# Kernel tuning notes

Measured on AMD Instinct MI355X. Metric: run time of the kernel, lower is better.

The kernel has to match this reference:

```python
import jax, jax.numpy as jnp
import numpy as np

B, T, V, H = 1, 1024, 32000, 2048
NH, NKV, HD = 8, 4, 256
QS, KVS = NH * HD, NKV * HD
I, L = 8192, 2
SCALE = 256.0 ** -0.5          # query_pre_attn_scalar ** -0.5
ATTN_CAP, FINAL_CAP = 50.0, 30.0
WIN, EPS, THETA = 512, 1e-6, 10000.0
NEG = -2.3819763e38


def setup_inputs() -> dict:
    key = jax.random.key(0)
    ks = jax.random.split(key, 12)
    s = 0.02
    return {
        "tokens": jax.random.randint(ks[0], (B, T), 0, V, dtype=jnp.int32),
        "embed": jax.random.normal(ks[1], (V, H), jnp.float32) * s,
        "qkv_w": jax.random.normal(ks[2], (L, (NH + 2 * NKV) * HD, H), jnp.float32) * s,
        "o_w": jax.random.normal(ks[3], (L, H, NH * HD), jnp.float32) * s,
        "gate_w": jax.random.normal(ks[4], (L, I, H), jnp.float32) * s,
        "up_w": jax.random.normal(ks[5], (L, I, H), jnp.float32) * s,
        "down_w": jax.random.normal(ks[6], (L, H, I), jnp.float32) * s,
        "ln_in": jax.random.normal(ks[7], (L, H), jnp.float32) * s,   # RMSNorm weight (zeros-init offset)
        "ln_pa": jax.random.normal(ks[8], (L, H), jnp.float32) * s,
        "ln_pre": jax.random.normal(ks[9], (L, H), jnp.float32) * s,
        "ln_post": jax.random.normal(ks[10], (L, H), jnp.float32) * s,
        "ln_f": jax.random.normal(ks[11], (H,), jnp.float32) * s,
    }


def rmsnorm(x, w):
    x = x.astype(jnp.float32)
    n = x * jax.lax.rsqrt(jnp.mean(x * x, axis=-1, keepdims=True) + EPS)
    return n * (1.0 + w)  # add_unit_offset=True


def rope(x, cos, sin):
    # x: [B, T, N, HD]; split-half complex rotary as in apply_rotary_emb
    x1, x2 = jnp.split(x, 2, axis=-1)
    c = cos[None, :, None, :]
    s = sin[None, :, None, :]
    return jnp.concatenate([x1 * c - x2 * s, x1 * s + x2 * c], axis=-1)


def reference(tokens, embed, qkv_w, o_w, gate_w, up_w, down_w,
              ln_in, ln_pa, ln_pre, ln_post, ln_f):
    pos = jnp.arange(T)
    inv = 1.0 / (THETA ** (jnp.arange(0, HD, 2, dtype=jnp.float32) / HD))  # [HD/2]
    ang = pos.astype(jnp.float32)[:, None] * inv[None, :]
    cos, sin = jnp.cos(ang), jnp.sin(ang)

    i, j = pos[:, None], pos[None, :]
    causal = j <= i
    mask_global = jnp.where(causal, 0.0, NEG).astype(jnp.float32)
    mask_local = jnp.where(causal & (i - j < WIN), 0.0, NEG).astype(jnp.float32)
    masks = [mask_local, mask_global]  # layer 0: LOCAL_SLIDING, layer 1: GLOBAL

    x = embed[tokens] * jnp.sqrt(jnp.float32(H))  # Gemma embedding normalizer

    for l in range(L):
        h = rmsnorm(x, ln_in[l])
        qkv = jnp.einsum('bth,oh->bto', h, qkv_w[l])
        q = qkv[..., :QS].reshape(B, T, NH, HD)
        k = qkv[..., QS:QS + KVS].reshape(B, T, NKV, HD)
        v = qkv[..., QS + KVS:].reshape(B, T, NKV, HD)
        q = rope(q, cos, sin)
        k = rope(k, cos, sin)
        # prefill: kv_write_indices=arange(T) -> cache == current k/v
        k = jnp.repeat(k, NH // NKV, axis=2)  # GQA repeat_interleave over heads
        v = jnp.repeat(v, NH // NKV, axis=2)
        scores = jnp.einsum('bqhd,bkhd->bhqk', q * SCALE, k)
        scores = jnp.tanh(scores / ATTN_CAP) * ATTN_CAP
        scores = scores + masks[l][None, None]
        attn = jax.nn.softmax(scores.astype(jnp.float32), axis=-1)
        out = jnp.einsum('bhqk,bkhd->bqhd', attn, v).reshape(B, T, NH * HD)
        out = jnp.einsum('bto,ho->bth', out, o_w[l])
        x = x + rmsnorm(out, ln_pa[l])

        h = rmsnorm(x, ln_pre[l])
        gate = jax.nn.gelu(jnp.einsum('bth,ih->bti', h, gate_w[l]), approximate=True)
        up = jnp.einsum('bth,ih->bti', h, up_w[l])
        ff = jnp.einsum('bti,hi->bth', gate * up, down_w[l])
        x = x + rmsnorm(ff, ln_post[l])

    x = rmsnorm(x, ln_f)
    logits = jnp.einsum('bth,vh->btv', x, embed)
    logits = jnp.tanh(logits / FINAL_CAP) * FINAL_CAP  # final_logit_softcapping
    return logits
```

## Files before the change

### kernel.cpp

```cpp
#include <hip/hip_runtime.h>
#include <hip/hip_bf16.h>
#include <math.h>

typedef unsigned short u16;
typedef __attribute__((ext_vector_type(8))) short bf16x8;
typedef __attribute__((ext_vector_type(4))) float f32x4;
typedef __attribute__((ext_vector_type(4))) u16 u16x4;

#define T_SEQ 1024
#define HDIM  2048
#define NHEAD 8
#define NKVH  4
#define HSZ   256
#define ISZ   8192
#define NVOC  32000

#define GLDS(src, dst) __builtin_amdgcn_global_load_lds( \
    (const __attribute__((address_space(1))) void*)(src), \
    (__attribute__((address_space(3))) void*)(dst), 16, 0, 0)

__device__ __forceinline__ u16 f2bf(float f) {
    union { float f; unsigned u; } v; v.f = f;
    return (u16)((v.u + 0x7fffu + ((v.u >> 16) & 1u)) >> 16);
}

__device__ __forceinline__ float fast_tanh(float x) {
    float e = __expf(-2.0f * fabsf(x));
    float t = (1.0f - e) / (1.0f + e);
    return copysignf(t, x);
}

__global__ __launch_bounds__(256)
void cvt_bf16(const float* __restrict__ s, u16* __restrict__ d, long n4)
{
    for (long i = blockIdx.x * 256L + threadIdx.x; i < n4; i += (long)gridDim.x * 256) {
        f32x4 v = ((const f32x4*)s)[i];
        u16x4 o;
        o.x = f2bf(v.x); o.y = f2bf(v.y); o.z = f2bf(v.z); o.w = f2bf(v.w);
        ((u16x4*)d)[i] = o;
    }
}

template<int EPI>
__global__ __launch_bounds__(512, 1)
void gemm_dp(const u16* __restrict__ A, int lda,
             const u16* __restrict__ B, int ldb,
             float* __restrict__ C, int ldc, long sC, int K)
{
    extern __shared__ u16 lds[];
    const int t = threadIdx.x;
    const int lane = t & 63, wid = t >> 6;
    const int z = blockIdx.z;
    A += (long)z * K;
    B += (long)z * K;
    C += (long)z * sC;

    const int nwg = gridDim.x * gridDim.y;
    int flat = blockIdx.y * gridDim.x + blockIdx.x;
    {
        const int q = nwg >> 3, r = nwg & 7;
        const int xcd = flat & 7, loc = flat >> 3;
        flat = (xcd < r ? xcd * (q + 1) : r * (q + 1) + (xcd - r) * q) + loc;
    }
    const int gm = gridDim.y;
    const long m0 = (long)(flat % gm) * 128;
    const long n0 = (long)(flat / gm) * 256;

    const int sr = t >> 3;
    const int sl = ((t & 7) ^ (sr & 7)) * 8;
    const u16* gA0 = A + (m0 + sr)       * (long)lda + sl;
    const u16* gA1 = A + (m0 + 64 + sr)  * (long)lda + sl;
    const u16* gB0 = B + (n0 + sr)       * (long)ldb + sl;
    const u16* gB1 = B + (n0 + 64 + sr)  * (long)ldb + sl;
    const u16* gB2 = B + (n0 + 128 + sr) * (long)ldb + sl;
    const u16* gB3 = B + (n0 + 192 + sr) * (long)ldb + sl;

    auto stage = [&](int kt) {
        const long ko = (long)kt * 64;
        char* d = (char*)lds + (kt % 3) * 49152 + t * 16;
        GLDS(gA0 + ko, d);
        GLDS(gA1 + ko, d + 8192);
        GLDS(gB0 + ko, d + 16384);
        GLDS(gB1 + ko, d + 24576);
        GLDS(gB2 + ko, d + 32768);
        GLDS(gB3 + ko, d + 40960);
    };

    f32x4 acc[4][4] = {};
    const int fr = lane & 15, kq = lane >> 4;
    const int wm = wid >> 2, wn = wid & 3;
    const int ps0 = ((kq)     ^ (lane & 7)) * 8;
    const int ps1 = ((4 + kq) ^ (lane & 7)) * 8;

    const int KT = K >> 6;
    stage(0);
    if (KT > 1) stage(1);
    if (KT > 2) stage(2);

    for (int kt = 0; kt < KT; ++kt) {
        if (kt < KT - 2)       asm volatile("s_waitcnt vmcnt(12)" ::: "memory");
        else if (kt == KT - 2) asm volatile("s_waitcnt vmcnt(6)" ::: "memory");
        else                   asm volatile("s_waitcnt vmcnt(0)" ::: "memory");
        __builtin_amdgcn_s_barrier();

        const u16* Asl = lds + (kt % 3) * 24576;
        const u16* Bsl = Asl + 8192;
        #pragma unroll
        for (int kk = 0; kk < 2; ++kk) {
            const int ps = kk ? ps1 : ps0;
            bf16x8 af[4], bfv[4];
            #pragma unroll
            for (int mi = 0; mi < 4; ++mi)
                af[mi] = *(const bf16x8*)(Asl + (wm * 64 + mi * 16 + fr) * 64 + ps);
            #pragma unroll
            for (int ni = 0; ni < 4; ++ni)
                bfv[ni] = *(const bf16x8*)(Bsl + (wn * 64 + ni * 16 + fr) * 64 + ps);
            #pragma unroll
            for (int mi = 0; mi < 4; ++mi)
                #pragma unroll
                for (int ni = 0; ni < 4; ++ni)
                    acc[mi][ni] = __builtin_amdgcn_mfma_f32_16x16x32_bf16(
                        af[mi], bfv[ni], acc[mi][ni], 0, 0, 0);
        }
        __builtin_amdgcn_s_barrier();
        if (kt + 3 < KT) stage(kt + 3);
    }

    const int crb = kq * 4, ccol = fr;
    #pragma unroll
    for (int mi = 0; mi < 4; ++mi) {
        #pragma unroll
        for (int rr = 0; rr < 4; ++rr) {
            const long row = m0 + wm * 64 + mi * 16 + crb + rr;
            float* cp = C + row * ldc + n0 + wn * 64 + ccol;
            #pragma unroll
            for (int ni = 0; ni < 4; ++ni) {
                float v = acc[mi][ni][rr];
                if (EPI == 1) v = fast_tanh(v * (1.0f / 30.0f)) * 30.0f;
                cp[ni * 16] = v;
            }
        }
    }
}

template<int EPI, typename CT>
__global__ __launch_bounds__(256)
void gemm_bt(const u16* __restrict__ A, int lda, long sA,
             const u16* __restrict__ B, int ldb, long sB, int bshift,
             CT* __restrict__ C, int ldc, long sC, int K)
{
    __shared__ u16 As[128 * 32];
    __shared__ u16 Bs[128 * 32];
    const int tid = threadIdx.x;
    const int lane = tid & 63, wid = tid >> 6;
    const int z = blockIdx.z;
    A += (long)z * sA;
    B += (long)(z >> bshift) * sB;
    C += (long)z * sC;

    const int nwg = gridDim.x * gridDim.y;
    int flat = blockIdx.y * gridDim.x + blockIdx.x;
    {
        const int q = nwg >> 3, r = nwg & 7;
        const int xcd = flat & 7, loc = flat >> 3;
        flat = (xcd < r ? xcd * (q + 1) : r * (q + 1) + (xcd - r) * q) + loc;
    }
    const int gm = gridDim.y;
    const long m0 = (long)(flat % gm) * 128;
    const long n0 = (long)(flat / gm) * 128;

    f32x4 acc[4][4] = {};

    const int ar = tid >> 2, ac = (tid & 3) * 8;
    const u16* gA0 = A + (m0 + ar) * lda + ac;
    const u16* gB0 = B + (n0 + ar) * (long)ldb + ac;
    const long a64 = 64L * lda, b64 = 64L * ldb;

    const int fr = lane & 15, fk = (lane >> 4) * 8;
    const int wm = (wid >> 1) * 64, wn = (wid & 1) * 64;

    for (int k0 = 0; k0 < K; k0 += 32) {
        GLDS(gA0 + k0,       &As[tid * 8]);
        GLDS(gA0 + a64 + k0, &As[2048 + tid * 8]);
        GLDS(gB0 + k0,       &Bs[tid * 8]);
        GLDS(gB0 + b64 + k0, &Bs[2048 + tid * 8]);
        __syncthreads();
        bf16x8 af[4], bfv[4];
        #pragma unroll
        for (int mi = 0; mi < 4; ++mi)
            af[mi] = *(const bf16x8*)(&As[(wm + mi * 16 + fr) * 32 + fk]);
        #pragma unroll
        for (int ni = 0; ni < 4; ++ni)
            bfv[ni] = *(const bf16x8*)(&Bs[(wn + ni * 16 + fr) * 32 + fk]);
        #pragma unroll
        for (int mi = 0; mi < 4; ++mi)
            #pragma unroll
            for (int ni = 0; ni < 4; ++ni)
                acc[mi][ni] = __builtin_amdgcn_mfma_f32_16x16x32_bf16(
                    af[mi], bfv[ni], acc[mi][ni], 0, 0, 0);
        __syncthreads();
    }

    const int crb = (lane >> 4) * 4, ccol = lane & 15;
    #pragma unroll
    for (int mi = 0; mi < 4; ++mi) {
        #pragma unroll
        for (int rr = 0; rr < 4; ++rr) {
            const long row = m0 + wm + mi * 16 + crb + rr;
            CT* cp = C + row * ldc + n0 + wn + ccol;
            #pragma unroll
            for (int ni = 0; ni < 4; ++ni) {
                float v = acc[mi][ni][rr];
                if (EPI == 1) v = fast_tanh(v * (1.0f / 30.0f)) * 30.0f;
                if constexpr (sizeof(CT) == 2) cp[ni * 16] = f2bf(v);
                else                           cp[ni * 16] = v;
            }
        }
    }
}

__global__ __launch_bounds__(256)
void embed_scale(const int* __restrict__ tok, const float* __restrict__ emb,
                 float* __restrict__ x)
{
    const int t = blockIdx.x, tid = threadIdx.x;
    const long src = (long)tok[t] * HDIM;
    f32x4 a = *(const f32x4*)(emb + src + tid * 8);
    f32x4 b = *(const f32x4*)(emb + src + tid * 8 + 4);
    a *= 45.254834f; b *= 45.254834f;
    *(f32x4*)(x + (long)t * HDIM + tid * 8) = a;
    *(f32x4*)(x + (long)t * HDIM + tid * 8 + 4) = b;
}

__device__ __forceinline__ float block_sum(float v, float* red) {
    #pragma unroll
    for (int o = 32; o; o >>= 1) v += __shfl_xor(v, o);
    const int tid = threadIdx.x;
    if ((tid & 63) == 0) red[tid >> 6] = v;
    __syncthreads();
    return red[0] + red[1] + red[2] + red[3];
}

__global__ __launch_bounds__(256)
void rmsnorm_bf16(const float* __restrict__ x, const float* __restrict__ w,
                  u16* __restrict__ out)
{
    __shared__ float red[4];
    const int t = blockIdx.x, tid = threadIdx.x;
    const float* row = x + (long)t * HDIM;
    f32x4 a = *(const f32x4*)(row + tid * 8);
    f32x4 b = *(const f32x4*)(row + tid * 8 + 4);
    float ss = a.x*a.x + a.y*a.y + a.z*a.z + a.w*a.w
             + b.x*b.x + b.y*b.y + b.z*b.z + b.w*b.w;
    ss = block_sum(ss, red);
    const float r = rsqrtf(ss * (1.0f / HDIM) + 1e-6f);
    f32x4 wa = *(const f32x4*)(w + tid * 8);
    f32x4 wb = *(const f32x4*)(w + tid * 8 + 4);
    u16x4 o0, o1;
    o0.x = f2bf(a.x * r * (1.0f + wa.x)); o0.y = f2bf(a.y * r * (1.0f + wa.y));
    o0.z = f2bf(a.z * r * (1.0f + wa.z)); o0.w = f2bf(a.w * r * (1.0f + wa.w));
    o1.x = f2bf(b.x * r * (1.0f + wb.x)); o1.y = f2bf(b.y * r * (1.0f + wb.y));
    o1.z = f2bf(b.z * r * (1.0f + wb.z)); o1.w = f2bf(b.w * r * (1.0f + wb.w));
    *(u16x4*)(out + (long)t * HDIM + tid * 8) = o0;
    *(u16x4*)(out + (long)t * HDIM + tid * 8 + 4) = o1;
}

__global__ __launch_bounds__(256)
void add_rmsnorm(float* __restrict__ x, const float* __restrict__ y,
                 const float* __restrict__ w, int nsplit, long stride)
{
    __shared__ float red[4];
    const int t = blockIdx.x, tid = threadIdx.x;
    const float* yr = y + (long)t * HDIM;
    f32x4 a = *(const f32x4*)(yr + tid * 8);
    f32x4 b = *(const f32x4*)(yr + tid * 8 + 4);
    for (int s = 1; s < nsplit; ++s) {
        a += *(const f32x4*)(yr + s * stride + tid * 8);
        b += *(const f32x4*)(yr + s * stride + tid * 8 + 4);
    }
    float ss = a.x*a.x + a.y*a.y + a.z*a.z + a.w*a.w
             + b.x*b.x + b.y*b.y + b.z*b.z + b.w*b.w;
    ss = block_sum(ss, red);
    const float r = rsqrtf(ss * (1.0f / HDIM) + 1e-6f);
    f32x4 wa = *(const f32x4*)(w + tid * 8);
    f32x4 wb = *(const f32x4*)(w + tid * 8 + 4);
    float* xr = x + (long)t * HDIM;
    f32x4 xa = *(const f32x4*)(xr + tid * 8);
    f32x4 xb = *(const f32x4*)(xr + tid * 8 + 4);
    xa.x += a.x * r * (1.0f + wa.x); xa.y += a.y * r * (1.0f + wa.y);
    xa.z += a.z * r * (1.0f + wa.z); xa.w += a.w * r * (1.0f + wa.w);
    xb.x += b.x * r * (1.0f + wb.x); xb.y += b.y * r * (1.0f + wb.y);
    xb.z += b.z * r * (1.0f + wb.z); xb.w += b.w * r * (1.0f + wb.w);
    *(f32x4*)(xr + tid * 8) = xa;
    *(f32x4*)(xr + tid * 8 + 4) = xb;
}

#define QKV_STRIDE (1024L * 4096)

__global__ __launch_bounds__(256)
void qkv_post(const float* __restrict__ qkv, u16* __restrict__ qb,
              u16* __restrict__ kb)
{
    const int t = blockIdx.x, tid = threadIdx.x;
    const float* row = qkv + (long)t * 4096;
    const float ft = (float)t;
    #pragma unroll
    for (int it = 0; it < 4; ++it) {
        const int p = tid + it * 256;
        const int nh = p >> 7, d = p & 127;
        const float inv = powf(10000.0f, -(float)d * (1.0f / 128.0f));
        const float ang = ft * inv;
        const float c = cosf(ang), s = sinf(ang);
        const int i1 = nh * 256 + d, i2 = i1 + 128;
        const float x1 = row[i1] + row[i1 + QKV_STRIDE];
        const float x2 = row[i2] + row[i2 + QKV_STRIDE];
        const long ob = ((long)nh * T_SEQ + t) * HSZ;
        qb[ob + d]       = f2bf((x1 * c - x2 * s) * 0.0625f);
        qb[ob + 128 + d] = f2bf((x1 * s + x2 * c) * 0.0625f);
    }
    #pragma unroll
    for (int it = 0; it < 2; ++it) {
        const int p = tid + it * 256;
        const int kv = p >> 7, d = p & 127;
        const float inv = powf(10000.0f, -(float)d * (1.0f / 128.0f));
        const float ang = ft * inv;
        const float c = cosf(ang), s = sinf(ang);
        const int i1 = 2048 + kv * 256 + d, i2 = i1 + 128;
        const float x1 = row[i1] + row[i1 + QKV_STRIDE];
        const float x2 = row[i2] + row[i2 + QKV_STRIDE];
        const long ob = ((long)kv * T_SEQ + t) * HSZ;
        kb[ob + d]       = f2bf(x1 * c - x2 * s);
        kb[ob + 128 + d] = f2bf(x1 * s + x2 * c);
    }
}

__global__ __launch_bounds__(256)
void v_transpose(const float* __restrict__ qkvb, u16* __restrict__ vT)
{
    __shared__ u16 tile[64][65];
    const int t0 = blockIdx.x * 64, d0 = blockIdx.y * 64, kv = blockIdx.z;
    const int lane = threadIdx.x & 63, w = threadIdx.x >> 6;
    #pragma unroll
    for (int i = 0; i < 16; ++i) {
        const int t = w * 16 + i;
        const long idx = (long)(t0 + t) * 4096 + 3072 + kv * 256 + d0 + lane;
        tile[t][lane] = f2bf(qkvb[idx] + qkvb[idx + QKV_STRIDE]);
    }
    __syncthreads();
    #pragma unroll
    for (int i = 0; i < 16; ++i) {
        const int d = w * 16 + i;
        vT[((long)kv * HSZ + d0 + d) * T_SEQ + t0 + lane] = tile[lane][d];
    }
}

__global__ __launch_bounds__(256)
void softmax_mask(const float* __restrict__ sc, u16* __restrict__ pr, int win)
{
    __shared__ float redm[4], reds[4];
    const int i = blockIdx.x, h = blockIdx.y, tid = threadIdx.x;
    const long base = ((long)h * T_SEQ + i) * T_SEQ;
    f32x4 sv = *(const f32x4*)(sc + base + tid * 4);
    float vals[4];
    #pragma unroll
    for (int j = 0; j < 4; ++j) {
        const int col = tid * 4 + j;
        const float s = fast_tanh(sv[j] * 0.02f) * 50.0f;
        const bool valid = (col <= i) && ((i - col) < win);
        vals[j] = valid ? s : -3.0e38f;
    }
    float m = fmaxf(fmaxf(vals[0], vals[1]), fmaxf(vals[2], vals[3]));
    #pragma unroll
    for (int o = 32; o; o >>= 1) m = fmaxf(m, __shfl_xor(m, o));
    if ((tid & 63) == 0) redm[tid >> 6] = m;
    __syncthreads();
    m = fmaxf(fmaxf(redm[0], redm[1]), fmaxf(redm[2], redm[3]));
    float sum = 0.0f;
    #pragma unroll
    for (int j = 0; j < 4; ++j) { vals[j] = __expf(vals[j] - m); sum += vals[j]; }
    #pragma unroll
    for (int o = 32; o; o >>= 1) sum += __shfl_xor(sum, o);
    if ((tid & 63) == 0) reds[tid >> 6] = sum;
    __syncthreads();
    sum = reds[0] + reds[1] + reds[2] + reds[3];
    const float inv = 1.0f / sum;
    u16x4 o4;
    #pragma unroll
    for (int j = 0; j < 4; ++j) o4[j] = f2bf(vals[j] * inv);
    *(u16x4*)(pr + base + tid * 4) = o4;
}

__global__ __launch_bounds__(256)
void mul_gelu(const float* __restrict__ g, const float* __restrict__ u,
              u16* __restrict__ p)
{
    const int n4 = (T_SEQ * ISZ) / 4;
    for (int i = blockIdx.x * 256 + threadIdx.x; i < n4; i += gridDim.x * 256) {
        f32x4 gv = ((const f32x4*)g)[i];
        f32x4 uv = ((const f32x4*)u)[i];
        u16x4 w;
        #pragma unroll
        for (int j = 0; j < 4; ++j) {
            const float xg = gv[j];
            const float tt = fast_tanh(0.79788456f * (xg + 0.044715f * xg * xg * xg));
            w[j] = f2bf(0.5f * xg * (1.0f + tt) * uv[j]);
        }
        ((u16x4*)p)[i] = w;
    }
}

extern "C" void kernel_launch(void* const* d_in, const int* in_sizes, int n_in,
                              void* d_out, int out_size, void* d_ws, size_t ws_size,
                              hipStream_t stream)
{
    (void)in_sizes; (void)n_in; (void)out_size; (void)ws_size;
    const int*   tokens = (const int*)  d_in[0];
    const float* emb    = (const float*)d_in[1];
    const float* qkv_w  = (const float*)d_in[2];
    const float* o_w    = (const float*)d_in[3];
    const float* gate_w = (const float*)d_in[4];
    const float* up_w   = (const float*)d_in[5];
    const float* down_w = (const float*)d_in[6];
    const float* ln_in  = (const float*)d_in[7];
    const float* ln_pa  = (const float*)d_in[8];
    const float* ln_pre = (const float*)d_in[9];
    const float* ln_post= (const float*)d_in[10];
    const float* ln_f   = (const float*)d_in[11];
    float* logits = (float*)d_out;

    char* base = (char*)d_ws;
    size_t off = 0;
    auto alloc = [&](size_t b) { char* p = base + off; off += (b + 255) & ~(size_t)255; return p; };

    float* x    = (float*)alloc((size_t)T_SEQ * HDIM * 4);
    u16*   hb   = (u16*)  alloc((size_t)T_SEQ * HDIM * 2);
    u16*   qb   = (u16*)  alloc((size_t)NHEAD * T_SEQ * HSZ * 2);
    u16*   kb   = (u16*)  alloc((size_t)NKVH * T_SEQ * HSZ * 2);
    u16*   vT   = (u16*)  alloc((size_t)NKVH * HSZ * T_SEQ * 2);
    u16*   ao   = (u16*)  alloc((size_t)T_SEQ * HDIM * 2);
    u16*   pb   = (u16*)  alloc((size_t)T_SEQ * ISZ * 2);
    char*  big  = alloc((size_t)2 * T_SEQ * ISZ * 4);
    float* P    = (float*)big;
    float* sc   = (float*)big;
    u16*   pr   = (u16*)(big + (size_t)NHEAD * T_SEQ * T_SEQ * 4);
    float* gb   = (float*)big;
    float* ub   = (float*)(big + (size_t)T_SEQ * ISZ * 4);
    u16*   wb   = (u16*)  alloc((size_t)NVOC * HDIM * 2);

    const size_t LDSB = 3 * 49152;
    const long s2048 = 1024L * 2048;

    embed_scale<<<T_SEQ, 256, 0, stream>>>(tokens, emb, x);
    for (int l = 0; l < 2; ++l) {
        rmsnorm_bf16<<<T_SEQ, 256, 0, stream>>>(x, ln_in + l * HDIM, hb);
        cvt_bf16<<<2048, 256, 0, stream>>>(qkv_w + (size_t)l * 4096 * HDIM, wb, 4096L * HDIM / 4);
        gemm_dp<0><<<dim3(16, 8, 2), 512, LDSB, stream>>>(
            hb, HDIM, wb, HDIM, P, 4096, QKV_STRIDE, 1024);
        qkv_post<<<T_SEQ, 256, 0, stream>>>(P, qb, kb);
        v_transpose<<<dim3(16, 4, 4), 256, 0, stream>>>(P, vT);
        gemm_bt<0, float><<<dim3(8, 8, NHEAD), 256, 0, stream>>>(
            qb, HSZ, (long)T_SEQ * HSZ, kb, HSZ, (long)T_SEQ * HSZ, 1,
            sc, T_SEQ, (long)T_SEQ * T_SEQ, HSZ);
        softmax_mask<<<dim3(T_SEQ, NHEAD, 1), 256, 0, stream>>>(
            sc, pr, l == 0 ? 512 : (1 << 30));
        gemm_bt<0, u16><<<dim3(2, 8, NHEAD), 256, 0, stream>>>(
            pr, T_SEQ, (long)T_SEQ * T_SEQ, vT, T_SEQ, (long)HSZ * T_SEQ, 1,
            ao, HDIM, (long)HSZ, T_SEQ);
        cvt_bf16<<<2048, 256, 0, stream>>>(o_w + (size_t)l * HDIM * HDIM, wb, (long)HDIM * HDIM / 4);
        gemm_dp<0><<<dim3(8, 8, 4), 512, LDSB, stream>>>(
            ao, HDIM, wb, HDIM, P, HDIM, s2048, 512);
        add_rmsnorm<<<T_SEQ, 256, 0, stream>>>(x, P, ln_pa + l * HDIM, 4, s2048);
        rmsnorm_bf16<<<T_SEQ, 256, 0, stream>>>(x, ln_pre + l * HDIM, hb);
        cvt_bf16<<<2048, 256, 0, stream>>>(gate_w + (size_t)l * ISZ * HDIM, wb, (long)ISZ * HDIM / 4);
        gemm_dp<0><<<dim3(32, 8, 1), 512, LDSB, stream>>>(
            hb, HDIM, wb, HDIM, gb, ISZ, 0, HDIM);
        cvt_bf16<<<2048, 256, 0, stream>>>(up_w + (size_t)l * ISZ * HDIM, wb, (long)ISZ * HDIM / 4);
        gemm_dp<0><<<dim3(32, 8, 1), 512, LDSB, stream>>>(
            hb, HDIM, wb, HDIM, ub, ISZ, 0, HDIM);
        mul_gelu<<<2048, 256, 0, stream>>>(gb, ub, pb);
        cvt_bf16<<<2048, 256, 0, stream>>>(down_w + (size_t)l * HDIM * ISZ, wb, (long)HDIM * ISZ / 4);
        gemm_dp<0><<<dim3(8, 8, 4), 512, LDSB, stream>>>(
            pb, ISZ, wb, ISZ, P, HDIM, s2048, 2048);
        add_rmsnorm<<<T_SEQ, 256, 0, stream>>>(x, P, ln_post + l * HDIM, 4, s2048);
    }
    rmsnorm_bf16<<<T_SEQ, 256, 0, stream>>>(x, ln_f, hb);
    cvt_bf16<<<2048, 256, 0, stream>>>(emb, wb, (long)NVOC * HDIM / 4);
    gemm_dp<1><<<dim3(125, 8, 1), 512, LDSB, stream>>>(
        hb, HDIM, wb, HDIM, logits, NVOC, 0, HDIM);
}
```

Before: 901.3 us.

## Fuse fp32-to-bf16 weight conversion into GEMM B-tile loading

Removes the separate cvt_bf16 passes over every weight matrix. The GEMM now loads fp32 B tiles into registers, packs them to bf16 with v_cvt_pk_bf16_f32, and writes them swizzled into LDS, while A tiles keep using global_load_lds. The pipeline drops from three LDS stages to two, with register double-buffering for B. This saves a full read and write of the weights per call, but each GEMM block now reads twice the B bytes and has a shallower pipeline with extra VGPR pressure.

Result: slower. 989.5 us (+9.8%).

```diff
diff --git a/kernel.cpp b/kernel.cpp
--- a/kernel.cpp
+++ b/kernel.cpp
@@ -6,6 +6,7 @@
 typedef __attribute__((ext_vector_type(8))) short bf16x8;
 typedef __attribute__((ext_vector_type(4))) float f32x4;
 typedef __attribute__((ext_vector_type(4))) u16 u16x4;
+typedef __attribute__((ext_vector_type(2))) unsigned u32x2;
 
 #define T_SEQ 1024
 #define HDIM  2048
@@ -24,27 +25,22 @@
     return (u16)((v.u + 0x7fffu + ((v.u >> 16) & 1u)) >> 16);
 }
 
+__device__ __forceinline__ unsigned cvt_pk_bf16(float a, float b) {
+    unsigned r;
+    asm("v_cvt_pk_bf16_f32 %0, %1, %2" : "=v"(r) : "v"(a), "v"(b));
+    return r;
+}
+
 __device__ __forceinline__ float fast_tanh(float x) {
     float e = __expf(-2.0f * fabsf(x));
     float t = (1.0f - e) / (1.0f + e);
     return copysignf(t, x);
 }
 
-__global__ __launch_bounds__(256)
-void cvt_bf16(const float* __restrict__ s, u16* __restrict__ d, long n4)
-{
-    for (long i = blockIdx.x * 256L + threadIdx.x; i < n4; i += (long)gridDim.x * 256) {
-        f32x4 v = ((const f32x4*)s)[i];
-        u16x4 o;
-        o.x = f2bf(v.x); o.y = f2bf(v.y); o.z = f2bf(v.z); o.w = f2bf(v.w);
-        ((u16x4*)d)[i] = o;
-    }
-}
-
 template<int EPI>
 __global__ __launch_bounds__(512, 1)
 void gemm_dp(const u16* __restrict__ A, int lda,
-             const u16* __restrict__ B, int ldb,
+             const float* __restrict__ B, int ldb,
              float* __restrict__ C, int ldc, long sC, int K)
 {
     extern __shared__ u16 lds[];
@@ -66,25 +62,14 @@
     const long m0 = (long)(flat % gm) * 128;
     const long n0 = (long)(flat / gm) * 256;
 
-    const int sr = t >> 3;
-    const int sl = ((t & 7) ^ (sr & 7)) * 8;
-    const u16* gA0 = A + (m0 + sr)       * (long)lda + sl;
-    const u16* gA1 = A + (m0 + 64 + sr)  * (long)lda + sl;
-    const u16* gB0 = B + (n0 + sr)       * (long)ldb + sl;
-    const u16* gB1 = B + (n0 + 64 + sr)  * (long)ldb + sl;
-    const u16* gB2 = B + (n0 + 128 + sr) * (long)ldb + sl;
-    const u16* gB3 = B + (n0 + 192 + sr) * (long)ldb + sl;
-
-    auto stage = [&](int kt) {
-        const long ko = (long)kt * 64;
-        char* d = (char*)lds + (kt % 3) * 49152 + t * 16;
-        GLDS(gA0 + ko, d);
-        GLDS(gA1 + ko, d + 8192);
-        GLDS(gB0 + ko, d + 16384);
-        GLDS(gB1 + ko, d + 24576);
-        GLDS(gB2 + ko, d + 32768);
-        GLDS(gB3 + ko, d + 40960);
-    };
+    const int asr = t >> 3;
+    const int asl = ((t & 7) ^ (asr & 7)) * 8;
+    const u16* gA0 = A + (m0 + asr)      * (long)lda + asl;
+    const u16* gA1 = A + (m0 + 64 + asr) * (long)lda + asl;
+
+    const float* gB = B + (n0 + (t >> 4)) * (long)ldb + (t & 15) * 4;
+    const long bstep = 32L * ldb;
+    const int boff = ((((t >> 1) & 7) ^ ((t >> 4) & 7)) << 4) + (t & 1) * 8;
 
     f32x4 acc[4][4] = {};
     const int fr = lane & 15, kq = lane >> 4;
@@ -93,17 +78,37 @@
     const int ps1 = ((4 + kq) ^ (lane & 7)) * 8;
 
     const int KT = K >> 6;
-    stage(0);
-    if (KT > 1) stage(1);
-    if (KT > 2) stage(2);
-
-    for (int kt = 0; kt < KT; ++kt) {
-        if (kt < KT - 2)       asm volatile("s_waitcnt vmcnt(12)" ::: "memory");
-        else if (kt == KT - 2) asm volatile("s_waitcnt vmcnt(6)" ::: "memory");
-        else                   asm volatile("s_waitcnt vmcnt(0)" ::: "memory");
+
+    auto stageA = [&](int kt) {
+        char* d = (char*)lds + (kt & 1) * 49152 + t * 16;
+        const long ko = (long)kt * 64;
+        GLDS(gA0 + ko, d);
+        GLDS(gA1 + ko, d + 8192);
+    };
+    auto loadB = [&](int kt, f32x4 (&R)[8]) {
+        const float* p = gB + (long)kt * 64;
+        #pragma unroll
+        for (int j = 0; j < 8; ++j) R[j] = *(const f32x4*)(p + j * bstep);
+    };
+    auto commitB = [&](int kt, f32x4 (&R)[8]) {
+        char* bb = (char*)lds + (kt & 1) * 49152 + 16384 + boff;
+        #pragma unroll
+        for (int j = 0; j < 8; ++j) {
+            u32x2 w;
+            w.x = cvt_pk_bf16(R[j].x, R[j].y);
+            w.y = cvt_pk_bf16(R[j].z, R[j].w);
+            *(u32x2*)(bb + (j * 32 + (t >> 4)) * 128) = w;
+        }
+    };
+    auto step = [&](int kt, f32x4 (&Rld)[8], f32x4 (&Rcm)[8]) {
+        if (kt + 1 < KT) asm volatile("s_waitcnt vmcnt(8)" ::: "memory");
+        else             asm volatile("s_waitcnt vmcnt(0)" ::: "memory");
+        asm volatile("s_waitcnt lgkmcnt(0)" ::: "memory");
         __builtin_amdgcn_s_barrier();
-
-        const u16* Asl = lds + (kt % 3) * 24576;
+        if (kt + 1 < KT) stageA(kt + 1);
+        if (kt + 2 < KT) loadB(kt + 2, Rld);
+
+        const u16* Asl = lds + (kt & 1) * 24576;
         const u16* Bsl = Asl + 8192;
         #pragma unroll
         for (int kk = 0; kk < 2; ++kk) {
@@ -122,8 +127,23 @@
                     acc[mi][ni] = __builtin_amdgcn_mfma_f32_16x16x32_bf16(
                         af[mi], bfv[ni], acc[mi][ni], 0, 0, 0);
         }
-        __builtin_amdgcn_s_barrier();
-        if (kt + 3 < KT) stage(kt + 3);
+        if (kt + 1 < KT) {
+            if (kt + 2 < KT) asm volatile("s_waitcnt vmcnt(10)" ::: "memory");
+            else             asm volatile("s_waitcnt vmcnt(2)" ::: "memory");
+            commitB(kt + 1, Rcm);
+        }
+    };
+
+    f32x4 R0[8], R1[8];
+    loadB(0, R0);
+    asm volatile("s_waitcnt vmcnt(0)" ::: "memory");
+    commitB(0, R0);
+    stageA(0);
+    loadB(1, R1);
+
+    for (int kt = 0; kt < KT; kt += 2) {
+        step(kt,     R0, R1);
+        step(kt + 1, R1, R0);
     }
 
     const int crb = kq * 4, ccol = fr;
@@ -445,17 +465,15 @@
     u16*   pr   = (u16*)(big + (size_t)NHEAD * T_SEQ * T_SEQ * 4);
     float* gb   = (float*)big;
     float* ub   = (float*)(big + (size_t)T_SEQ * ISZ * 4);
-    u16*   wb   = (u16*)  alloc((size_t)NVOC * HDIM * 2);
-
-    const size_t LDSB = 3 * 49152;
+
+    const size_t LDSB = 2 * 49152;
     const long s2048 = 1024L * 2048;
 
     embed_scale<<<T_SEQ, 256, 0, stream>>>(tokens, emb, x);
     for (int l = 0; l < 2; ++l) {
         rmsnorm_bf16<<<T_SEQ, 256, 0, stream>>>(x, ln_in + l * HDIM, hb);
-        cvt_bf16<<<2048, 256, 0, stream>>>(qkv_w + (size_t)l * 4096 * HDIM, wb, 4096L * HDIM / 4);
         gemm_dp<0><<<dim3(16, 8, 2), 512, LDSB, stream>>>(
-            hb, HDIM, wb, HDIM, P, 4096, QKV_STRIDE, 1024);
+            hb, HDIM, qkv_w + (size_t)l * 4096 * HDIM, HDIM, P, 4096, QKV_STRIDE, 1024);
         qkv_post<<<T_SEQ, 256, 0, stream>>>(P, qb, kb);
         v_transpose<<<dim3(16, 4, 4), 256, 0, stream>>>(P, vT);
         gemm_bt<0, float><<<dim3(8, 8, NHEAD), 256, 0, stream>>>(
@@ -466,25 +484,20 @@
         gemm_bt<0, u16><<<dim3(2, 8, NHEAD), 256, 0, stream>>>(
             pr, T_SEQ, (long)T_SEQ * T_SEQ, vT, T_SEQ, (long)HSZ * T_SEQ, 1,
             ao, HDIM, (long)HSZ, T_SEQ);
-        cvt_bf16<<<2048, 256, 0, stream>>>(o_w + (size_t)l * HDIM * HDIM, wb, (long)HDIM * HDIM / 4);
         gemm_dp<0><<<dim3(8, 8, 4), 512, LDSB, stream>>>(
-            ao, HDIM, wb, HDIM, P, HDIM, s2048, 512);
+            ao, HDIM, o_w + (size_t)l * HDIM * HDIM, HDIM, P, HDIM, s2048, 512);
         add_rmsnorm<<<T_SEQ, 256, 0, stream>>>(x, P, ln_pa + l * HDIM, 4, s2048);
         rmsnorm_bf16<<<T_SEQ, 256, 0, stream>>>(x, ln_pre + l * HDIM, hb);
-        cvt_bf16<<<2048, 256, 0, stream>>>(gate_w + (size_t)l * ISZ * HDIM, wb, (long)ISZ * HDIM / 4);
         gemm_dp<0><<<dim3(32, 8, 1), 512, LDSB, stream>>>(
-            hb, HDIM, wb, HDIM, gb, ISZ, 0, HDIM);
-        cvt_bf16<<<2048, 256, 0, stream>>>(up_w + (size_t)l * ISZ * HDIM, wb, (long)ISZ * HDIM / 4);
+            hb, HDIM, gate_w + (size_t)l * ISZ * HDIM, HDIM, gb, ISZ, 0, HDIM);
         gemm_dp<0><<<dim3(32, 8, 1), 512, LDSB, stream>>>(
-            hb, HDIM, wb, HDIM, ub, ISZ, 0, HDIM);
+            hb, HDIM, up_w + (size_t)l * ISZ * HDIM, HDIM, ub, ISZ, 0, HDIM);
         mul_gelu<<<2048, 256, 0, stream>>>(gb, ub, pb);
-        cvt_bf16<<<2048, 256, 0, stream>>>(down_w + (size_t)l * HDIM * ISZ, wb, (long)HDIM * ISZ / 4);
         gemm_dp<0><<<dim3(8, 8, 4), 512, LDSB, stream>>>(
-            pb, ISZ, wb, ISZ, P, HDIM, s2048, 2048);
+            pb, ISZ, down_w + (size_t)l * HDIM * ISZ, ISZ, P, HDIM, s2048, 2048);
         add_rmsnorm<<<T_SEQ, 256, 0, stream>>>(x, P, ln_post + l * HDIM, 4, s2048);
     }
     rmsnorm_bf16<<<T_SEQ, 256, 0, stream>>>(x, ln_f, hb);
-    cvt_bf16<<<2048, 256, 0, stream>>>(emb, wb, (long)NVOC * HDIM / 4);
     gemm_dp<1><<<dim3(125, 8, 1), 512, LDSB, stream>>>(
-        hb, HDIM, wb, HDIM, logits, NVOC, 0, HDIM);
-}
+        hb, HDIM, emb, HDIM, logits, NVOC, 0, HDIM);
+}
```

## Switch GEMMs to 256x256 tiles with interleaved 8-wave schedule and more split-K

Applied to the files above, without the earlier changes.

Replaces the 128x256 triple-buffered GEMM with a 256x256 double-buffered kernel that interleaves LDS fragment loads, global-to-LDS prefetch and MFMA clusters in four phases per K step, using barriers and s_setprio. Split-K factors are raised for the QKV, o-proj, down-proj and gate/up GEMMs to keep enough workgroups, with the reduction kernels summing 4 or 8 slices. The gate/up elementwise step is split into gelu_reduce and mul_reduce so both can reuse the single scratch buffer. The aim is higher arithmetic intensity per tile and better MFMA issue; the cost is extra split-K partial traffic and an intermediate bf16 rounding of the gelu output.

After: 1.004 ms. +11.4%, slower.

```diff
diff --git a/kernel.cpp b/kernel.cpp
--- a/kernel.cpp
+++ b/kernel.cpp
@@ -23,11 +23,18 @@
     union { float f; unsigned u; } v; v.f = f;
     return (u16)((v.u + 0x7fffu + ((v.u >> 16) & 1u)) >> 16);
 }
+__device__ __forceinline__ float bf2f(u16 h) {
+    union { unsigned u; float f; } v; v.u = (unsigned)h << 16; return v.f;
+}
 
 __device__ __forceinline__ float fast_tanh(float x) {
     float e = __expf(-2.0f * fabsf(x));
     float t = (1.0f - e) / (1.0f + e);
     return copysignf(t, x);
+}
+
+__device__ __forceinline__ f32x4 mfma16(bf16x8 a, bf16x8 b, f32x4 c) {
+    return __builtin_amdgcn_mfma_f32_16x16x32_bf16(a, b, c, 0, 0, 0);
 }
 
 __global__ __launch_bounds__(256)
@@ -43,9 +50,9 @@
 
 template<int EPI>
 __global__ __launch_bounds__(512, 1)
-void gemm_dp(const u16* __restrict__ A, int lda,
-             const u16* __restrict__ B, int ldb,
-             float* __restrict__ C, int ldc, long sC, int K)
+void gemm8(const u16* __restrict__ A, int lda,
+           const u16* __restrict__ B, int ldb,
+           float* __restrict__ C, int ldc, long sC, int K)
 {
     extern __shared__ u16 lds[];
     const int t = threadIdx.x;
@@ -63,79 +70,129 @@
         flat = (xcd < r ? xcd * (q + 1) : r * (q + 1) + (xcd - r) * q) + loc;
     }
     const int gm = gridDim.y;
-    const long m0 = (long)(flat % gm) * 128;
+    const long m0 = (long)(flat % gm) * 256;
     const long n0 = (long)(flat / gm) * 256;
 
     const int sr = t >> 3;
     const int sl = ((t & 7) ^ (sr & 7)) * 8;
-    const u16* gA0 = A + (m0 + sr)       * (long)lda + sl;
-    const u16* gA1 = A + (m0 + 64 + sr)  * (long)lda + sl;
-    const u16* gB0 = B + (n0 + sr)       * (long)ldb + sl;
-    const u16* gB1 = B + (n0 + 64 + sr)  * (long)ldb + sl;
-    const u16* gB2 = B + (n0 + 128 + sr) * (long)ldb + sl;
-    const u16* gB3 = B + (n0 + 192 + sr) * (long)ldb + sl;
-
-    auto stage = [&](int kt) {
-        const long ko = (long)kt * 64;
-        char* d = (char*)lds + (kt % 3) * 49152 + t * 16;
-        GLDS(gA0 + ko, d);
-        GLDS(gA1 + ko, d + 8192);
-        GLDS(gB0 + ko, d + 16384);
-        GLDS(gB1 + ko, d + 24576);
-        GLDS(gB2 + ko, d + 32768);
-        GLDS(gB3 + ko, d + 40960);
+    const u16* gA = A + (m0 + sr) * (long)lda + sl;
+    const u16* gB = B + (n0 + sr) * (long)ldb + sl;
+
+    auto stA = [&](int kt, int ro) {
+        char* d = (char*)lds + (kt & 1) * 65536 + ro * 128 + t * 16;
+        GLDS(gA + (long)ro * lda + (long)kt * 64, d);
     };
-
-    f32x4 acc[4][4] = {};
+    auto stB = [&](int kt, int ro) {
+        char* d = (char*)lds + (kt & 1) * 65536 + 32768 + ro * 128 + t * 16;
+        GLDS(gB + (long)ro * ldb + (long)kt * 64, d);
+    };
+
+    f32x4 acc[8][4] = {};
     const int fr = lane & 15, kq = lane >> 4;
     const int wm = wid >> 2, wn = wid & 3;
-    const int ps0 = ((kq)     ^ (lane & 7)) * 8;
-    const int ps1 = ((4 + kq) ^ (lane & 7)) * 8;
-
+    const int g0 = ((kq) ^ (lane & 7)) * 8;
+    const int g1 = ((4 + kq) ^ (lane & 7)) * 8;
     const int KT = K >> 6;
-    stage(0);
-    if (KT > 1) stage(1);
-    if (KT > 2) stage(2);
+
+    stA(0, 0); stA(0, 64); stA(0, 128); stA(0, 192);
+    stB(0, 0); stB(0, 64); stB(0, 128); stB(0, 192);
+    stA(1, 0); stA(1, 64); stA(1, 128); stA(1, 192);
+    stB(1, 0); stB(1, 64); stB(1, 128); stB(1, 192);
+    asm volatile("s_waitcnt vmcnt(8)" ::: "memory");
+    __builtin_amdgcn_s_barrier();
 
     for (int kt = 0; kt < KT; ++kt) {
-        if (kt < KT - 2)       asm volatile("s_waitcnt vmcnt(12)" ::: "memory");
-        else if (kt == KT - 2) asm volatile("s_waitcnt vmcnt(6)" ::: "memory");
-        else                   asm volatile("s_waitcnt vmcnt(0)" ::: "memory");
-        __builtin_amdgcn_s_barrier();
-
-        const u16* Asl = lds + (kt % 3) * 24576;
-        const u16* Bsl = Asl + 8192;
-        #pragma unroll
-        for (int kk = 0; kk < 2; ++kk) {
-            const int ps = kk ? ps1 : ps0;
-            bf16x8 af[4], bfv[4];
-            #pragma unroll
-            for (int mi = 0; mi < 4; ++mi)
-                af[mi] = *(const bf16x8*)(Asl + (wm * 64 + mi * 16 + fr) * 64 + ps);
-            #pragma unroll
-            for (int ni = 0; ni < 4; ++ni)
-                bfv[ni] = *(const bf16x8*)(Bsl + (wn * 64 + ni * 16 + fr) * 64 + ps);
-            #pragma unroll
-            for (int mi = 0; mi < 4; ++mi)
-                #pragma unroll
-                for (int ni = 0; ni < 4; ++ni)
-                    acc[mi][ni] = __builtin_amdgcn_mfma_f32_16x16x32_bf16(
-                        af[mi], bfv[ni], acc[mi][ni], 0, 0, 0);
-        }
-        __builtin_amdgcn_s_barrier();
-        if (kt + 3 < KT) stage(kt + 3);
+        const u16* As = lds + (kt & 1) * 32768;
+        const u16* Bs = As + 16384;
+        const int arow = wm * 128 + fr;
+        const int brow = wn * 64 + fr;
+        bf16x8 aL[4][2], aH[4][2], bL[2][2], bH[2][2];
+
+        #pragma unroll
+        for (int mi = 0; mi < 4; ++mi) {
+            aL[mi][0] = *(const bf16x8*)(As + (arow + mi * 16) * 64 + g0);
+            aL[mi][1] = *(const bf16x8*)(As + (arow + mi * 16) * 64 + g1);
+        }
+        #pragma unroll
+        for (int ni = 0; ni < 2; ++ni) {
+            bL[ni][0] = *(const bf16x8*)(Bs + (brow + ni * 16) * 64 + g0);
+            bL[ni][1] = *(const bf16x8*)(Bs + (brow + ni * 16) * 64 + g1);
+        }
+        __builtin_amdgcn_s_barrier();
+        __builtin_amdgcn_s_setprio(1);
+        #pragma unroll
+        for (int mi = 0; mi < 4; ++mi)
+            #pragma unroll
+            for (int ni = 0; ni < 2; ++ni) {
+                acc[mi][ni] = mfma16(aL[mi][0], bL[ni][0], acc[mi][ni]);
+                acc[mi][ni] = mfma16(aL[mi][1], bL[ni][1], acc[mi][ni]);
+            }
+        __builtin_amdgcn_s_setprio(0);
+        __builtin_amdgcn_s_barrier();
+
+        #pragma unroll
+        for (int ni = 0; ni < 2; ++ni) {
+            bH[ni][0] = *(const bf16x8*)(Bs + (brow + (ni + 2) * 16) * 64 + g0);
+            bH[ni][1] = *(const bf16x8*)(Bs + (brow + (ni + 2) * 16) * 64 + g1);
+        }
+        __builtin_amdgcn_s_barrier();
+        __builtin_amdgcn_s_setprio(1);
+        #pragma unroll
+        for (int mi = 0; mi < 4; ++mi)
+            #pragma unroll
+            for (int ni = 0; ni < 2; ++ni) {
+                acc[mi][ni + 2] = mfma16(aL[mi][0], bH[ni][0], acc[mi][ni + 2]);
+                acc[mi][ni + 2] = mfma16(aL[mi][1], bH[ni][1], acc[mi][ni + 2]);
+            }
+        __builtin_amdgcn_s_setprio(0);
+        __builtin_amdgcn_s_barrier();
+
+        #pragma unroll
+        for (int mi = 0; mi < 4; ++mi) {
+            aH[mi][0] = *(const bf16x8*)(As + (arow + (mi + 4) * 16) * 64 + g0);
+            aH[mi][1] = *(const bf16x8*)(As + (arow + (mi + 4) * 16) * 64 + g1);
+        }
+        if (kt + 2 < KT) { stB(kt + 2, 0); stB(kt + 2, 64); stB(kt + 2, 128); stB(kt + 2, 192); }
+        __builtin_amdgcn_s_barrier();
+        __builtin_amdgcn_s_setprio(1);
+        #pragma unroll
+        for (int mi = 0; mi < 4; ++mi)
+            #pragma unroll
+            for (int ni = 0; ni < 2; ++ni) {
+                acc[mi + 4][ni] = mfma16(aH[mi][0], bL[ni][0], acc[mi + 4][ni]);
+                acc[mi + 4][ni] = mfma16(aH[mi][1], bL[ni][1], acc[mi + 4][ni]);
+            }
+        __builtin_amdgcn_s_setprio(0);
+        __builtin_amdgcn_s_barrier();
+
+        if (kt + 2 < KT) { stA(kt + 2, 0); stA(kt + 2, 64); stA(kt + 2, 128); stA(kt + 2, 192); }
+        __builtin_amdgcn_s_barrier();
+        __builtin_amdgcn_s_setprio(1);
+        #pragma unroll
+        for (int mi = 0; mi < 4; ++mi)
+            #pragma unroll
+            for (int ni = 0; ni < 2; ++ni) {
+                acc[mi + 4][ni + 2] = mfma16(aH[mi][0], bH[ni][0], acc[mi + 4][ni + 2]);
+                acc[mi + 4][ni + 2] = mfma16(aH[mi][1], bH[ni][1], acc[mi + 4][ni + 2]);
+            }
+        __builtin_amdgcn_s_setprio(0);
+        if (kt + 1 < KT) {
+            if (kt + 2 < KT) asm volatile("s_waitcnt vmcnt(8)" ::: "memory");
+            else             asm volatile("s_waitcnt vmcnt(0)" ::: "memory");
+            __builtin_amdgcn_s_barrier();
+        }
     }
 
     const int crb = kq * 4, ccol = fr;
     #pragma unroll
-    for (int mi = 0; mi < 4; ++mi) {
+    for (int mj = 0; mj < 8; ++mj) {
         #pragma unroll
         for (int rr = 0; rr < 4; ++rr) {
-            const long row = m0 + wm * 64 + mi * 16 + crb + rr;
+            const long row = m0 + wm * 128 + mj * 16 + crb + rr;
             float* cp = C + row * ldc + n0 + wn * 64 + ccol;
             #pragma unroll
             for (int ni = 0; ni < 4; ++ni) {
-                float v = acc[mi][ni][rr];
+                float v = acc[mj][ni][rr];
                 if (EPI == 1) v = fast_tanh(v * (1.0f / 30.0f)) * 30.0f;
                 cp[ni * 16] = v;
             }
@@ -196,8 +253,7 @@
         for (int mi = 0; mi < 4; ++mi)
             #pragma unroll
             for (int ni = 0; ni < 4; ++ni)
-                acc[mi][ni] = __builtin_amdgcn_mfma_f32_16x16x32_bf16(
-                    af[mi], bfv[ni], acc[mi][ni], 0, 0, 0);
+                acc[mi][ni] = mfma16(af[mi], bfv[ni], acc[mi][ni]);
         __syncthreads();
     }
 
@@ -312,8 +368,12 @@
         const float ang = ft * inv;
         const float c = cosf(ang), s = sinf(ang);
         const int i1 = nh * 256 + d, i2 = i1 + 128;
-        const float x1 = row[i1] + row[i1 + QKV_STRIDE];
-        const float x2 = row[i2] + row[i2 + QKV_STRIDE];
+        float x1 = 0.0f, x2 = 0.0f;
+        #pragma unroll
+        for (int sl = 0; sl < 4; ++sl) {
+            x1 += row[i1 + sl * QKV_STRIDE];
+            x2 += row[i2 + sl * QKV_STRIDE];
+        }
         const long ob = ((long)nh * T_SEQ + t) * HSZ;
         qb[ob + d]       = f2bf((x1 * c - x2 * s) * 0.0625f);
         qb[ob + 128 + d] = f2bf((x1 * s + x2 * c) * 0.0625f);
@@ -326,8 +386,12 @@
         const float ang = ft * inv;
         const float c = cosf(ang), s = sinf(ang);
         const int i1 = 2048 + kv * 256 + d, i2 = i1 + 128;
-        const float x1 = row[i1] + row[i1 + QKV_STRIDE];
-        const float x2 = row[i2] + row[i2 + QKV_STRIDE];
+        float x1 = 0.0f, x2 = 0.0f;
+        #pragma unroll
+        for (int sl = 0; sl < 4; ++sl) {
+            x1 += row[i1 + sl * QKV_STRIDE];
+            x2 += row[i2 + sl * QKV_STRIDE];
+        }
         const long ob = ((long)kv * T_SEQ + t) * HSZ;
         kb[ob + d]       = f2bf(x1 * c - x2 * s);
         kb[ob + 128 + d] = f2bf(x1 * s + x2 * c);
@@ -344,7 +408,10 @@
     for (int i = 0; i < 16; ++i) {
         const int t = w * 16 + i;
         const long idx = (long)(t0 + t) * 4096 + 3072 + kv * 256 + d0 + lane;
-        tile[t][lane] = f2bf(qkvb[idx] + qkvb[idx + QKV_STRIDE]);
+        float v = 0.0f;
+        #pragma unroll
+        for (int sl = 0; sl < 4; ++sl) v += qkvb[idx + sl * QKV_STRIDE];
+        tile[t][lane] = f2bf(v);
     }
     __syncthreads();
     #pragma unroll
@@ -390,21 +457,35 @@
     *(u16x4*)(pr + base + tid * 4) = o4;
 }
 
-__global__ __launch_bounds__(256)
-void mul_gelu(const float* __restrict__ g, const float* __restrict__ u,
-              u16* __restrict__ p)
-{
-    const int n4 = (T_SEQ * ISZ) / 4;
-    for (int i = blockIdx.x * 256 + threadIdx.x; i < n4; i += gridDim.x * 256) {
-        f32x4 gv = ((const f32x4*)g)[i];
-        f32x4 uv = ((const f32x4*)u)[i];
+#define GUP_S4 (1024L * 8192 / 4)
+
+__global__ __launch_bounds__(256)
+void gelu_reduce(const float* __restrict__ g, u16* __restrict__ p)
+{
+    const long n4 = (long)T_SEQ * ISZ / 4;
+    for (long i = blockIdx.x * 256L + threadIdx.x; i < n4; i += (long)gridDim.x * 256) {
+        f32x4 gv = ((const f32x4*)g)[i] + ((const f32x4*)g)[i + GUP_S4];
         u16x4 w;
         #pragma unroll
         for (int j = 0; j < 4; ++j) {
             const float xg = gv[j];
             const float tt = fast_tanh(0.79788456f * (xg + 0.044715f * xg * xg * xg));
-            w[j] = f2bf(0.5f * xg * (1.0f + tt) * uv[j]);
-        }
+            w[j] = f2bf(0.5f * xg * (1.0f + tt));
+        }
+        ((u16x4*)p)[i] = w;
+    }
+}
+
+__global__ __launch_bounds__(256)
+void mul_reduce(const float* __restrict__ u, u16* __restrict__ p)
+{
+    const long n4 = (long)T_SEQ * ISZ / 4;
+    for (long i = blockIdx.x * 256L + threadIdx.x; i < n4; i += (long)gridDim.x * 256) {
+        f32x4 uv = ((const f32x4*)u)[i] + ((const f32x4*)u)[i + GUP_S4];
+        u16x4 pv = ((const u16x4*)p)[i];
+        u16x4 w;
+        #pragma unroll
+        for (int j = 0; j < 4; ++j) w[j] = f2bf(bf2f(pv[j]) * uv[j]);
         ((u16x4*)p)[i] = w;
     }
 }
@@ -443,19 +524,18 @@
     float* P    = (float*)big;
     float* sc   = (float*)big;
     u16*   pr   = (u16*)(big + (size_t)NHEAD * T_SEQ * T_SEQ * 4);
-    float* gb   = (float*)big;
-    float* ub   = (float*)(big + (size_t)T_SEQ * ISZ * 4);
     u16*   wb   = (u16*)  alloc((size_t)NVOC * HDIM * 2);
 
-    const size_t LDSB = 3 * 49152;
+    const size_t LDS8 = 2 * 65536;
     const long s2048 = 1024L * 2048;
+    const long s8192 = 1024L * 8192;
 
     embed_scale<<<T_SEQ, 256, 0, stream>>>(tokens, emb, x);
     for (int l = 0; l < 2; ++l) {
         rmsnorm_bf16<<<T_SEQ, 256, 0, stream>>>(x, ln_in + l * HDIM, hb);
         cvt_bf16<<<2048, 256, 0, stream>>>(qkv_w + (size_t)l * 4096 * HDIM, wb, 4096L * HDIM / 4);
-        gemm_dp<0><<<dim3(16, 8, 2), 512, LDSB, stream>>>(
-            hb, HDIM, wb, HDIM, P, 4096, QKV_STRIDE, 1024);
+        gemm8<0><<<dim3(16, 4, 4), 512, LDS8, stream>>>(
+            hb, HDIM, wb, HDIM, P, 4096, QKV_STRIDE, 512);
         qkv_post<<<T_SEQ, 256, 0, stream>>>(P, qb, kb);
         v_transpose<<<dim3(16, 4, 4), 256, 0, stream>>>(P, vT);
         gemm_bt<0, float><<<dim3(8, 8, NHEAD), 256, 0, stream>>>(
@@ -467,24 +547,25 @@
             pr, T_SEQ, (long)T_SEQ * T_SEQ, vT, T_SEQ, (long)HSZ * T_SEQ, 1,
             ao, HDIM, (long)HSZ, T_SEQ);
         cvt_bf16<<<2048, 256, 0, stream>>>(o_w + (size_t)l * HDIM * HDIM, wb, (long)HDIM * HDIM / 4);
-        gemm_dp<0><<<dim3(8, 8, 4), 512, LDSB, stream>>>(
-            ao, HDIM, wb, HDIM, P, HDIM, s2048, 512);
-        add_rmsnorm<<<T_SEQ, 256, 0, stream>>>(x, P, ln_pa + l * HDIM, 4, s2048);
+        gemm8<0><<<dim3(8, 4, 8), 512, LDS8, stream>>>(
+            ao, HDIM, wb, HDIM, P, HDIM, s2048, 256);
+        add_rmsnorm<<<T_SEQ, 256, 0, stream>>>(x, P, ln_pa + l * HDIM, 8, s2048);
         rmsnorm_bf16<<<T_SEQ, 256, 0, stream>>>(x, ln_pre + l * HDIM, hb);
         cvt_bf16<<<2048, 256, 0, stream>>>(gate_w + (size_t)l * ISZ * HDIM, wb, (long)ISZ * HDIM / 4);
-        gemm_dp<0><<<dim3(32, 8, 1), 512, LDSB, stream>>>(
-            hb, HDIM, wb, HDIM, gb, ISZ, 0, HDIM);
+        gemm8<0><<<dim3(32, 4, 2), 512, LDS8, stream>>>(
+            hb, HDIM, wb, HDIM, P, ISZ, s8192, 1024);
+        gelu_reduce<<<2048, 256, 0, stream>>>(P, pb);
         cvt_bf16<<<2048, 256, 0, stream>>>(up_w + (size_t)l * ISZ * HDIM, wb, (long)ISZ * HDIM / 4);
-        gemm_dp<0><<<dim3(32, 8, 1), 512, LDSB, stream>>>(
-            hb, HDIM, wb, HDIM, ub, ISZ, 0, HDIM);
-        mul_gelu<<<2048, 256, 0, stream>>>(gb, ub, pb);
+        gemm8<0><<<dim3(32, 4, 2), 512, LDS8, stream>>>(
+            hb, HDIM, wb, HDIM, P, ISZ, s8192, 1024);
+        mul_reduce<<<2048, 256, 0, stream>>>(P, pb);
         cvt_bf16<<<2048, 256, 0, stream>>>(down_w + (size_t)l * HDIM * ISZ, wb, (long)HDIM * ISZ / 4);
-        gemm_dp<0><<<dim3(8, 8, 4), 512, LDSB, stream>>>(
-            pb, ISZ, wb, ISZ, P, HDIM, s2048, 2048);
-        add_rmsnorm<<<T_SEQ, 256, 0, stream>>>(x, P, ln_post + l * HDIM, 4, s2048);
+        gemm8<0><<<dim3(8, 4, 8), 512, LDS8, stream>>>(
+            pb, ISZ, wb, ISZ, P, HDIM, s2048, 1024);
+        add_rmsnorm<<<T_SEQ, 256, 0, stream>>>(x, P, ln_post + l * HDIM, 8, s2048);
     }
     rmsnorm_bf16<<<T_SEQ, 256, 0, stream>>>(x, ln_f, hb);
     cvt_bf16<<<2048, 256, 0, stream>>>(emb, wb, (long)NVOC * HDIM / 4);
-    gemm_dp<1><<<dim3(125, 8, 1), 512, LDSB, stream>>>(
+    gemm8<1><<<dim3(125, 4, 1), 512, LDS8, stream>>>(
         hb, HDIM, wb, HDIM, logits, NVOC, 0, HDIM);
 }
```
